# Performance work log

Hardware: AMD Instinct MI355X
Metric: run time of the kernel (lower is better)

## Reference

```python
import jax, jax.numpy as jnp
import numpy as np

N_NODES = 100000
N_EDGES = 1600000
IN_C = 128
HID = 128
LAT = 64
N_LAYERS = 3
N_GRAPHS = 1000


def setup_inputs() -> dict:
    key = jax.random.key(0)
    ks = jax.random.split(key, 16)
    x = jax.random.normal(ks[0], (N_NODES, IN_C), dtype=jnp.float32)
    edge_index = jax.random.randint(ks[1], (2, N_EDGES), 0, N_NODES, dtype=jnp.int64)
    batch = jnp.sort(jax.random.randint(ks[2], (N_NODES,), 0, N_GRAPHS, dtype=jnp.int64))
    s = 1.0 / np.sqrt(HID)
    # per-layer GIN MLP params (in_c == hidden for all layers since IN_C == HID)
    W1 = jax.random.normal(ks[3], (N_LAYERS, IN_C, HID), dtype=jnp.float32) * s
    b1 = jnp.zeros((N_LAYERS, HID), dtype=jnp.float32)
    W2 = jax.random.normal(ks[4], (N_LAYERS, HID, HID), dtype=jnp.float32) * s
    b2 = jnp.zeros((N_LAYERS, HID), dtype=jnp.float32)
    W_mu = jax.random.normal(ks[5], (HID, LAT), dtype=jnp.float32) * s
    b_mu = jnp.zeros((LAT,), dtype=jnp.float32)
    W_lv = jax.random.normal(ks[6], (HID, LAT), dtype=jnp.float32) * s
    b_lv = jnp.zeros((LAT,), dtype=jnp.float32)
    return {"x": x, "edge_index": edge_index, "batch": batch,
            "W1": W1, "b1": b1, "W2": W2, "b2": b2,
            "W_mu": W_mu, "b_mu": b_mu, "W_lv": W_lv, "b_lv": b_lv}


def reference(x, edge_index, batch, W1, b1, W2, b2, W_mu, b_mu, W_lv, b_lv):
    src, dst = edge_index[0], edge_index[1]
    h = x
    for i in range(N_LAYERS):
        # GINConv (eps=0): h' = MLP(h + sum_{j in N(i)} h_j); scatter-add over edges
        agg = h + jax.ops.segment_sum(h[src], dst, num_segments=N_NODES)
        h = jax.nn.relu(agg @ W1[i] + b1[i])
        h = jax.nn.relu(h @ W2[i] + b2[i])
        h = jax.nn.relu(h)  # extra ReLU in forward after conv (idempotent here)
    # global_add_pool: segment-sum nodes into graphs
    g = jax.ops.segment_sum(h, batch, num_segments=N_GRAPHS)  # [G, HID]
    mu = g @ W_mu + b_mu
    logvar = g @ W_lv + b_lv
    return (mu, logvar)
```

## Files before the change

kernel.cpp:

```cpp
#include <hip/hip_runtime.h>

#define N_NODES 100000
#define N_EDGES 1600000
#define HID 128
#define LAT 64
#define N_LAYERS 3
#define N_GRAPHS 1000
#define CAP 64
#define NBIN 391
#define MAXBIN 4608
#define ACHUNK 8192
#define ABLOCKS ((N_EDGES + ACHUNK - 1) / ACHUNK)
#define CVT_BLOCKS (N_NODES * HID / 4 / 256)

typedef short bf16x8 __attribute__((ext_vector_type(8)));
typedef float f32x4 __attribute__((ext_vector_type(4)));

__device__ __forceinline__ float bf2f(unsigned short h) {
    union { unsigned int u; float f; } c;
    c.u = ((unsigned int)h) << 16;
    return c.f;
}
__device__ __forceinline__ unsigned short f2bf(float f) {
    union { float f; unsigned int u; } c;
    c.f = f;
    unsigned int u = c.u;
    return (unsigned short)((u + 0x7fffu + ((u >> 16) & 1u)) >> 16);
}
__device__ __forceinline__ unsigned int pack2(float a, float b) {
    return (unsigned int)f2bf(a) | ((unsigned int)f2bf(b) << 16);
}
__device__ __forceinline__ void addrow(float* acc, uint4 w) {
    acc[0] += bf2f((unsigned short)w.x); acc[1] += bf2f((unsigned short)(w.x >> 16));
    acc[2] += bf2f((unsigned short)w.y); acc[3] += bf2f((unsigned short)(w.y >> 16));
    acc[4] += bf2f((unsigned short)w.z); acc[5] += bf2f((unsigned short)(w.z >> 16));
    acc[6] += bf2f((unsigned short)w.w); acc[7] += bf2f((unsigned short)(w.w >> 16));
}

__global__ __launch_bounds__(256) void prep_kernel(const float* __restrict__ x,
                                                   unsigned short* __restrict__ xb,
                                                   const float* __restrict__ W1,
                                                   const float* __restrict__ W2,
                                                   unsigned short* __restrict__ Wt) {
    int blk = blockIdx.x;
    if (blk < 6) {
        const float* W = ((blk & 1) ? W2 : W1) + (size_t)(blk >> 1) * HID * HID;
        unsigned short* D = Wt + (size_t)blk * HID * HID;
        for (int idx = threadIdx.x; idx < HID * HID; idx += 256) {
            int n = idx >> 7, k = idx & 127;
            D[n * HID + k] = f2bf(W[k * HID + n]);
        }
        return;
    }
    int i = (blk - 6) * 256 + threadIdx.x;
    if (i >= N_NODES * HID / 4) return;
    float4 v = ((const float4*)x)[i];
    ((uint2*)xb)[i] = make_uint2(pack2(v.x, v.y), pack2(v.z, v.w));
}

__global__ __launch_bounds__(256) void binA_kernel(const int* __restrict__ ei,
                                                   int* __restrict__ gcnt,
                                                   unsigned int* __restrict__ ebin) {
    __shared__ unsigned int scount[NBIN];
    __shared__ unsigned int sfill[NBIN];
    int t = threadIdx.x;
    int base = blockIdx.x * ACHUNK;
    int n = N_EDGES - base;
    if (n > ACHUNK) n = ACHUNK;
    for (int i = t; i < NBIN; i += 256) scount[i] = 0u;
    __syncthreads();
    for (int i = t; i < n; i += 256) {
        int d = ei[N_EDGES + base + i];
        atomicAdd(&scount[d >> 8], 1u);
    }
    __syncthreads();
    for (int b = t; b < NBIN; b += 256) {
        unsigned int c = scount[b];
        sfill[b] = c ? (unsigned int)atomicAdd(&gcnt[b], (int)c) : 0u;
    }
    __syncthreads();
    for (int i = t; i < n; i += 256) {
        int s = ei[base + i];
        int d = ei[N_EDGES + base + i];
        int b = d >> 8;
        unsigned int pos = atomicAdd(&sfill[b], 1u);
        ebin[(size_t)b * MAXBIN + pos] = ((unsigned int)(d & 255) << 24) | (unsigned int)s;
    }
}

__global__ __launch_bounds__(256) void binB_kernel(const unsigned int* __restrict__ ebin,
                                                   const int* __restrict__ gcnt,
                                                   int* __restrict__ cnt,
                                                   int* __restrict__ csr) {
    __shared__ int scnt[256];
    int b = blockIdx.x;
    int t = threadIdx.x;
    scnt[t] = 0;
    __syncthreads();
    int n0 = b << 8;
    int c = gcnt[b];
    const unsigned int* src = ebin + (size_t)b * MAXBIN;
    for (int i = t; i < c; i += 256) {
        unsigned int e = src[i];
        int dl = (int)(e >> 24);
        int slot = atomicAdd(&scnt[dl], 1);
        csr[(size_t)(n0 + dl) * CAP + slot] = (int)(e & 0xFFFFFFu);
    }
    __syncthreads();
    int node = n0 + t;
    if (node < N_NODES) cnt[node] = scnt[t];
}

__global__ __launch_bounds__(256) void fused_kernel(const unsigned short* __restrict__ h,
                                                    const int* __restrict__ cnt,
                                                    const int* __restrict__ csr,
                                                    const unsigned short* __restrict__ W1t,
                                                    const float* __restrict__ b1,
                                                    const unsigned short* __restrict__ W2t,
                                                    const float* __restrict__ b2,
                                                    unsigned short* __restrict__ out,
                                                    const int* __restrict__ batch,
                                                    float* __restrict__ gpool) {
    __shared__ unsigned short sA[64][136];
    __shared__ unsigned short sW[128][40];
    __shared__ float sb[128];
    __shared__ int sbatch[64];
    const int t = threadIdx.x;
    const int w = t >> 6;
    const int l = t & 63;
    const int lm = l & 15;
    const int quad = l >> 4;
    const int row0 = blockIdx.x * 64;

    if (gpool && t < 64) {
        int n = row0 + t;
        sbatch[t] = (n < N_NODES) ? batch[n] : -1;
    }

    {
        const int q = t & 15;
        const int g16 = t >> 4;
        for (int r4 = 0; r4 < 4; ++r4) {
            int rloc = (r4 << 4) + g16;
            int node = row0 + rloc;
            float acc[8] = {0.f, 0.f, 0.f, 0.f, 0.f, 0.f, 0.f, 0.f};
            if (node < N_NODES) {
                addrow(acc, *(const uint4*)(h + (size_t)node * HID + q * 8));
                const int* nl = csr + (size_t)node * CAP;
                int deg = cnt[node];
                int e = 0;
                for (; e + 8 <= deg; e += 8) {
                    int s0 = nl[e], s1 = nl[e + 1], s2 = nl[e + 2], s3 = nl[e + 3];
                    int s4 = nl[e + 4], s5 = nl[e + 5], s6 = nl[e + 6], s7 = nl[e + 7];
                    uint4 w0 = *(const uint4*)(h + (size_t)s0 * HID + q * 8);
                    uint4 w1 = *(const uint4*)(h + (size_t)s1 * HID + q * 8);
                    uint4 w2 = *(const uint4*)(h + (size_t)s2 * HID + q * 8);
                    uint4 w3 = *(const uint4*)(h + (size_t)s3 * HID + q * 8);
                    uint4 w4 = *(const uint4*)(h + (size_t)s4 * HID + q * 8);
                    uint4 w5 = *(const uint4*)(h + (size_t)s5 * HID + q * 8);
                    uint4 w6 = *(const uint4*)(h + (size_t)s6 * HID + q * 8);
                    uint4 w7 = *(const uint4*)(h + (size_t)s7 * HID + q * 8);
                    addrow(acc, w0); addrow(acc, w1); addrow(acc, w2); addrow(acc, w3);
                    addrow(acc, w4); addrow(acc, w5); addrow(acc, w6); addrow(acc, w7);
                }
                for (; e + 4 <= deg; e += 4) {
                    int s0 = nl[e], s1 = nl[e + 1], s2 = nl[e + 2], s3 = nl[e + 3];
                    uint4 w0 = *(const uint4*)(h + (size_t)s0 * HID + q * 8);
                    uint4 w1 = *(const uint4*)(h + (size_t)s1 * HID + q * 8);
                    uint4 w2 = *(const uint4*)(h + (size_t)s2 * HID + q * 8);
                    uint4 w3 = *(const uint4*)(h + (size_t)s3 * HID + q * 8);
                    addrow(acc, w0); addrow(acc, w1); addrow(acc, w2); addrow(acc, w3);
                }
                for (; e < deg; ++e) {
                    addrow(acc, *(const uint4*)(h + (size_t)nl[e] * HID + q * 8));
                }
            }
            uint4 o;
            o.x = pack2(acc[0], acc[1]);
            o.y = pack2(acc[2], acc[3]);
            o.z = pack2(acc[4], acc[5]);
            o.w = pack2(acc[6], acc[7]);
            *(uint4*)&sA[rloc][q * 8] = o;
        }
    }

    const unsigned short* Wt[2] = {W1t, W2t};
    const float* bias[2] = {b1, b2};

    for (int p = 0; p < 2; ++p) {
        if (t < 128) sb[t] = bias[p][t];
        f32x4 acc[8];
#pragma unroll
        for (int nt = 0; nt < 8; ++nt) acc[nt] = (f32x4){0.f, 0.f, 0.f, 0.f};

        for (int kc = 0; kc < 4; ++kc) {
            __syncthreads();
            for (int idx = t; idx < 512; idx += 256) {
                int n = idx >> 2, kq = idx & 3;
                *(uint4*)&sW[n][kq * 8] =
                    *(const uint4*)(Wt[p] + (size_t)n * HID + kc * 32 + kq * 8);
            }
            __syncthreads();
            bf16x8 a = *(const bf16x8*)&sA[w * 16 + lm][kc * 32 + quad * 8];
#pragma unroll
            for (int nt = 0; nt < 8; ++nt) {
                bf16x8 b = *(const bf16x8*)&sW[nt * 16 + lm][quad * 8];
                acc[nt] = __builtin_amdgcn_mfma_f32_16x16x32_bf16(a, b, acc[nt], 0, 0, 0);
            }
        }
        __syncthreads();
#pragma unroll
        for (int nt = 0; nt < 8; ++nt) {
            float bv = sb[nt * 16 + lm];
#pragma unroll
            for (int r = 0; r < 4; ++r) {
                int m = w * 16 + quad * 4 + r;
                float val = fmaxf(acc[nt][r] + bv, 0.f);
                sA[m][nt * 16 + lm] = f2bf(val);
            }
        }
        __syncthreads();
    }

    if (!gpool) {
        for (int idx = t; idx < 1024; idx += 256) {
            int r = idx >> 4, c = idx & 15;
            int grow = row0 + r;
            if (grow < N_NODES)
                *(uint4*)(out + (size_t)grow * HID + c * 8) = *(const uint4*)&sA[r][c * 8];
        }
    } else {
        int c = t & 127;
        int r0 = (t >> 7) * 32;
        float acc = 0.f;
        int cur = sbatch[r0];
        for (int r = r0; r < r0 + 32; ++r) {
            int b = sbatch[r];
            if (b < 0) break;
            if (b != cur) {
                atomicAdd(&gpool[(size_t)cur * HID + c], acc);
                acc = 0.f;
                cur = b;
            }
            acc += bf2f(sA[r][c]);
        }
        if (cur >= 0) atomicAdd(&gpool[(size_t)cur * HID + c], acc);
    }
}

__global__ __launch_bounds__(128) void head_kernel(const float* __restrict__ g,
                                                   const float* __restrict__ Wmu,
                                                   const float* __restrict__ bmu,
                                                   const float* __restrict__ Wlv,
                                                   const float* __restrict__ blv,
                                                   float* __restrict__ out) {
    __shared__ float sg[HID];
    int gi = blockIdx.x;
    sg[threadIdx.x] = g[(size_t)gi * HID + threadIdx.x];
    __syncthreads();
    int j = threadIdx.x & 63;
    bool is_lv = threadIdx.x >= 64;
    const float* W = is_lv ? Wlv : Wmu;
    float acc = is_lv ? blv[j] : bmu[j];
    for (int k = 0; k < HID; ++k) acc = fmaf(sg[k], W[k * LAT + j], acc);
    out[(is_lv ? (size_t)N_GRAPHS * LAT : 0) + (size_t)gi * LAT + j] = acc;
}

extern "C" void kernel_launch(void* const* d_in, const int* in_sizes, int n_in,
                              void* d_out, int out_size, void* d_ws, size_t ws_size,
                              hipStream_t stream) {
    const float* x     = (const float*)d_in[0];
    const int*   ei    = (const int*)d_in[1];
    const int*   batch = (const int*)d_in[2];
    const float* W1    = (const float*)d_in[3];
    const float* b1    = (const float*)d_in[4];
    const float* W2    = (const float*)d_in[5];
    const float* b2    = (const float*)d_in[6];
    const float* Wmu   = (const float*)d_in[7];
    const float* bmu   = (const float*)d_in[8];
    const float* Wlv   = (const float*)d_in[9];
    const float* blv   = (const float*)d_in[10];
    float* out = (float*)d_out;

    unsigned short* xb   = (unsigned short*)d_ws;
    unsigned short* h1   = xb + (size_t)N_NODES * HID;
    unsigned short* h2   = h1 + (size_t)N_NODES * HID;
    int* csr = (int*)(h2 + (size_t)N_NODES * HID);
    unsigned int* ebin = (unsigned int*)(csr + (size_t)N_NODES * CAP);
    unsigned short* Wt = (unsigned short*)(ebin + (size_t)NBIN * MAXBIN);
    float* g  = (float*)(Wt + (size_t)6 * HID * HID);
    int* gcnt = (int*)(g + (size_t)N_GRAPHS * HID);
    int* cnt  = gcnt + NBIN + 1;

    hipMemsetAsync(g, 0, (size_t)N_GRAPHS * HID * sizeof(float) + (NBIN + 1) * sizeof(int),
                   stream);

    binA_kernel<<<ABLOCKS, 256, 0, stream>>>(ei, gcnt, ebin);
    binB_kernel<<<NBIN, 256, 0, stream>>>(ebin, gcnt, cnt, csr);

    prep_kernel<<<CVT_BLOCKS + 6, 256, 0, stream>>>(x, xb, W1, W2, Wt);

    const unsigned short* hcur = xb;
    unsigned short* hdst = h1;
    for (int i = 0; i < N_LAYERS; ++i) {
        bool last = (i == N_LAYERS - 1);
        fused_kernel<<<(N_NODES + 63) / 64, 256, 0, stream>>>(
            hcur, cnt, csr,
            Wt + (size_t)(2 * i) * HID * HID, b1 + (size_t)i * HID,
            Wt + (size_t)(2 * i + 1) * HID * HID, b2 + (size_t)i * HID,
            hdst, batch, last ? g : nullptr);
        hcur = hdst;
        hdst = (hdst == h1) ? h2 : h1;
    }
    head_kernel<<<N_GRAPHS, 128, 0, stream>>>(g, Wmu, bmu, Wlv, blv, out);
}
```

Before: 454.5 us.

## Shrink fused GIN tile to 16 rows, read weights from global, merge setup kernels

The fused aggregation+MLP kernel now handles 16 nodes per block instead of 64. Each wave computes two 16-column output tiles and loads its MFMA B fragments straight from global/L2, dropping the shared-memory weight staging and most barriers. This gives far more blocks for latency hiding in the gather phase, at the cost of more redundant weight reads per node. Separately, the prep (conversion/transpose) work is folded into the edge-binning kernel launch to save one launch and let the two run concurrently.

```diff
diff --git a/kernel.cpp b/kernel.cpp
--- a/kernel.cpp
+++ b/kernel.cpp
@@ -37,34 +37,36 @@
     acc[6] += bf2f((unsigned short)w.w); acc[7] += bf2f((unsigned short)(w.w >> 16));
 }
 
-__global__ __launch_bounds__(256) void prep_kernel(const float* __restrict__ x,
-                                                   unsigned short* __restrict__ xb,
-                                                   const float* __restrict__ W1,
-                                                   const float* __restrict__ W2,
-                                                   unsigned short* __restrict__ Wt) {
-    int blk = blockIdx.x;
-    if (blk < 6) {
-        const float* W = ((blk & 1) ? W2 : W1) + (size_t)(blk >> 1) * HID * HID;
-        unsigned short* D = Wt + (size_t)blk * HID * HID;
-        for (int idx = threadIdx.x; idx < HID * HID; idx += 256) {
-            int n = idx >> 7, k = idx & 127;
-            D[n * HID + k] = f2bf(W[k * HID + n]);
-        }
-        return;
-    }
-    int i = (blk - 6) * 256 + threadIdx.x;
-    if (i >= N_NODES * HID / 4) return;
-    float4 v = ((const float4*)x)[i];
-    ((uint2*)xb)[i] = make_uint2(pack2(v.x, v.y), pack2(v.z, v.w));
-}
-
-__global__ __launch_bounds__(256) void binA_kernel(const int* __restrict__ ei,
-                                                   int* __restrict__ gcnt,
-                                                   unsigned int* __restrict__ ebin) {
+__global__ __launch_bounds__(256) void setup_kernel(const int* __restrict__ ei,
+                                                    int* __restrict__ gcnt,
+                                                    unsigned int* __restrict__ ebin,
+                                                    const float* __restrict__ x,
+                                                    unsigned short* __restrict__ xb,
+                                                    const float* __restrict__ W1,
+                                                    const float* __restrict__ W2,
+                                                    unsigned short* __restrict__ Wt) {
     __shared__ unsigned int scount[NBIN];
     __shared__ unsigned int sfill[NBIN];
     int t = threadIdx.x;
-    int base = blockIdx.x * ACHUNK;
+    int blk = blockIdx.x;
+    if (blk >= ABLOCKS) {
+        int b2 = blk - ABLOCKS;
+        if (b2 < 6) {
+            const float* W = ((b2 & 1) ? W2 : W1) + (size_t)(b2 >> 1) * HID * HID;
+            unsigned short* D = Wt + (size_t)b2 * HID * HID;
+            for (int idx = t; idx < HID * HID; idx += 256) {
+                int n = idx >> 7, k = idx & 127;
+                D[n * HID + k] = f2bf(W[k * HID + n]);
+            }
+            return;
+        }
+        int i = (b2 - 6) * 256 + t;
+        if (i >= N_NODES * HID / 4) return;
+        float4 v = ((const float4*)x)[i];
+        ((uint2*)xb)[i] = make_uint2(pack2(v.x, v.y), pack2(v.z, v.w));
+        return;
+    }
+    int base = blk * ACHUNK;
     int n = N_EDGES - base;
     if (n > ACHUNK) n = ACHUNK;
     for (int i = t; i < NBIN; i += 256) scount[i] = 0u;
@@ -121,120 +123,105 @@
                                                     unsigned short* __restrict__ out,
                                                     const int* __restrict__ batch,
                                                     float* __restrict__ gpool) {
-    __shared__ unsigned short sA[64][136];
-    __shared__ unsigned short sW[128][40];
-    __shared__ float sb[128];
-    __shared__ int sbatch[64];
+    __shared__ unsigned short sA[16][136];
+    __shared__ int sbatch[16];
     const int t = threadIdx.x;
     const int w = t >> 6;
     const int l = t & 63;
     const int lm = l & 15;
     const int quad = l >> 4;
-    const int row0 = blockIdx.x * 64;
-
-    if (gpool && t < 64) {
+    const int row0 = blockIdx.x * 16;
+
+    if (gpool && t < 16) {
         int n = row0 + t;
         sbatch[t] = (n < N_NODES) ? batch[n] : -1;
     }
 
     {
         const int q = t & 15;
-        const int g16 = t >> 4;
-        for (int r4 = 0; r4 < 4; ++r4) {
-            int rloc = (r4 << 4) + g16;
-            int node = row0 + rloc;
-            float acc[8] = {0.f, 0.f, 0.f, 0.f, 0.f, 0.f, 0.f, 0.f};
-            if (node < N_NODES) {
-                addrow(acc, *(const uint4*)(h + (size_t)node * HID + q * 8));
-                const int* nl = csr + (size_t)node * CAP;
-                int deg = cnt[node];
-                int e = 0;
-                for (; e + 8 <= deg; e += 8) {
-                    int s0 = nl[e], s1 = nl[e + 1], s2 = nl[e + 2], s3 = nl[e + 3];
-                    int s4 = nl[e + 4], s5 = nl[e + 5], s6 = nl[e + 6], s7 = nl[e + 7];
-                    uint4 w0 = *(const uint4*)(h + (size_t)s0 * HID + q * 8);
-                    uint4 w1 = *(const uint4*)(h + (size_t)s1 * HID + q * 8);
-                    uint4 w2 = *(const uint4*)(h + (size_t)s2 * HID + q * 8);
-                    uint4 w3 = *(const uint4*)(h + (size_t)s3 * HID + q * 8);
-                    uint4 w4 = *(const uint4*)(h + (size_t)s4 * HID + q * 8);
-                    uint4 w5 = *(const uint4*)(h + (size_t)s5 * HID + q * 8);
-                    uint4 w6 = *(const uint4*)(h + (size_t)s6 * HID + q * 8);
-                    uint4 w7 = *(const uint4*)(h + (size_t)s7 * HID + q * 8);
-                    addrow(acc, w0); addrow(acc, w1); addrow(acc, w2); addrow(acc, w3);
-                    addrow(acc, w4); addrow(acc, w5); addrow(acc, w6); addrow(acc, w7);
-                }
-                for (; e + 4 <= deg; e += 4) {
-                    int s0 = nl[e], s1 = nl[e + 1], s2 = nl[e + 2], s3 = nl[e + 3];
-                    uint4 w0 = *(const uint4*)(h + (size_t)s0 * HID + q * 8);
-                    uint4 w1 = *(const uint4*)(h + (size_t)s1 * HID + q * 8);
-                    uint4 w2 = *(const uint4*)(h + (size_t)s2 * HID + q * 8);
-                    uint4 w3 = *(const uint4*)(h + (size_t)s3 * HID + q * 8);
-                    addrow(acc, w0); addrow(acc, w1); addrow(acc, w2); addrow(acc, w3);
-                }
-                for (; e < deg; ++e) {
-                    addrow(acc, *(const uint4*)(h + (size_t)nl[e] * HID + q * 8));
-                }
-            }
-            uint4 o;
-            o.x = pack2(acc[0], acc[1]);
-            o.y = pack2(acc[2], acc[3]);
-            o.z = pack2(acc[4], acc[5]);
-            o.w = pack2(acc[6], acc[7]);
-            *(uint4*)&sA[rloc][q * 8] = o;
-        }
-    }
-
-    const unsigned short* Wt[2] = {W1t, W2t};
+        const int rloc = t >> 4;
+        int node = row0 + rloc;
+        float acc[8] = {0.f, 0.f, 0.f, 0.f, 0.f, 0.f, 0.f, 0.f};
+        if (node < N_NODES) {
+            addrow(acc, *(const uint4*)(h + (size_t)node * HID + q * 8));
+            const int* nl = csr + (size_t)node * CAP;
+            int deg = cnt[node];
+            int e = 0;
+            for (; e + 8 <= deg; e += 8) {
+                int s0 = nl[e], s1 = nl[e + 1], s2 = nl[e + 2], s3 = nl[e + 3];
+                int s4 = nl[e + 4], s5 = nl[e + 5], s6 = nl[e + 6], s7 = nl[e + 7];
+                uint4 w0 = *(const uint4*)(h + (size_t)s0 * HID + q * 8);
+                uint4 w1 = *(const uint4*)(h + (size_t)s1 * HID + q * 8);
+                uint4 w2 = *(const uint4*)(h + (size_t)s2 * HID + q * 8);
+                uint4 w3 = *(const uint4*)(h + (size_t)s3 * HID + q * 8);
+                uint4 w4 = *(const uint4*)(h + (size_t)s4 * HID + q * 8);
+                uint4 w5 = *(const uint4*)(h + (size_t)s5 * HID + q * 8);
+                uint4 w6 = *(const uint4*)(h + (size_t)s6 * HID + q * 8);
+                uint4 w7 = *(const uint4*)(h + (size_t)s7 * HID + q * 8);
+                addrow(acc, w0); addrow(acc, w1); addrow(acc, w2); addrow(acc, w3);
+                addrow(acc, w4); addrow(acc, w5); addrow(acc, w6); addrow(acc, w7);
+            }
+            for (; e + 4 <= deg; e += 4) {
+                int s0 = nl[e], s1 = nl[e + 1], s2 = nl[e + 2], s3 = nl[e + 3];
+                uint4 w0 = *(const uint4*)(h + (size_t)s0 * HID + q * 8);
+                uint4 w1 = *(const uint4*)(h + (size_t)s1 * HID + q * 8);
+                uint4 w2 = *(const uint4*)(h + (size_t)s2 * HID + q * 8);
+                uint4 w3 = *(const uint4*)(h + (size_t)s3 * HID + q * 8);
+                addrow(acc, w0); addrow(acc, w1); addrow(acc, w2); addrow(acc, w3);
+            }
+            for (; e < deg; ++e) {
+                addrow(acc, *(const uint4*)(h + (size_t)nl[e] * HID + q * 8));
+            }
+        }
+        uint4 o;
+        o.x = pack2(acc[0], acc[1]);
+        o.y = pack2(acc[2], acc[3]);
+        o.z = pack2(acc[4], acc[5]);
+        o.w = pack2(acc[6], acc[7]);
+        *(uint4*)&sA[rloc][q * 8] = o;
+    }
+    __syncthreads();
+
+    const unsigned short* Wt2[2] = {W1t, W2t};
     const float* bias[2] = {b1, b2};
+    const int n0a = (2 * w) * 16 + lm;
+    const int n0b = (2 * w + 1) * 16 + lm;
 
     for (int p = 0; p < 2; ++p) {
-        if (t < 128) sb[t] = bias[p][t];
-        f32x4 acc[8];
+        f32x4 acc0 = (f32x4){0.f, 0.f, 0.f, 0.f};
+        f32x4 acc1 = (f32x4){0.f, 0.f, 0.f, 0.f};
+        const unsigned short* Wp = Wt2[p];
 #pragma unroll
-        for (int nt = 0; nt < 8; ++nt) acc[nt] = (f32x4){0.f, 0.f, 0.f, 0.f};
-
         for (int kc = 0; kc < 4; ++kc) {
-            __syncthreads();
-            for (int idx = t; idx < 512; idx += 256) {
-                int n = idx >> 2, kq = idx & 3;
-                *(uint4*)&sW[n][kq * 8] =
-                    *(const uint4*)(Wt[p] + (size_t)n * HID + kc * 32 + kq * 8);
-            }
-            __syncthreads();
-            bf16x8 a = *(const bf16x8*)&sA[w * 16 + lm][kc * 32 + quad * 8];
+            bf16x8 a = *(const bf16x8*)&sA[lm][kc * 32 + quad * 8];
+            bf16x8 bfr0 = *(const bf16x8*)(Wp + (size_t)n0a * HID + kc * 32 + quad * 8);
+            bf16x8 bfr1 = *(const bf16x8*)(Wp + (size_t)n0b * HID + kc * 32 + quad * 8);
+            acc0 = __builtin_amdgcn_mfma_f32_16x16x32_bf16(a, bfr0, acc0, 0, 0, 0);
+            acc1 = __builtin_amdgcn_mfma_f32_16x16x32_bf16(a, bfr1, acc1, 0, 0, 0);
+        }
+        __syncthreads();
+        float bv0 = bias[p][n0a];
+        float bv1 = bias[p][n0b];
 #pragma unroll
-            for (int nt = 0; nt < 8; ++nt) {
-                bf16x8 b = *(const bf16x8*)&sW[nt * 16 + lm][quad * 8];
-                acc[nt] = __builtin_amdgcn_mfma_f32_16x16x32_bf16(a, b, acc[nt], 0, 0, 0);
-            }
+        for (int r = 0; r < 4; ++r) {
+            int m = quad * 4 + r;
+            sA[m][n0a] = f2bf(fmaxf(acc0[r] + bv0, 0.f));
+            sA[m][n0b] = f2bf(fmaxf(acc1[r] + bv1, 0.f));
         }
         __syncthreads();
-#pragma unroll
-        for (int nt = 0; nt < 8; ++nt) {
-            float bv = sb[nt * 16 + lm];
-#pragma unroll
-            for (int r = 0; r < 4; ++r) {
-                int m = w * 16 + quad * 4 + r;
-                float val = fmaxf(acc[nt][r] + bv, 0.f);
-                sA[m][nt * 16 + lm] = f2bf(val);
-            }
-        }
-        __syncthreads();
     }
 
     if (!gpool) {
-        for (int idx = t; idx < 1024; idx += 256) {
-            int r = idx >> 4, c = idx & 15;
-            int grow = row0 + r;
-            if (grow < N_NODES)
-                *(uint4*)(out + (size_t)grow * HID + c * 8) = *(const uint4*)&sA[r][c * 8];
-        }
+        int r = t >> 4, c = t & 15;
+        int grow = row0 + r;
+        if (grow < N_NODES)
+            *(uint4*)(out + (size_t)grow * HID + c * 8) = *(const uint4*)&sA[r][c * 8];
     } else {
         int c = t & 127;
-        int r0 = (t >> 7) * 32;
+        int r0 = (t >> 7) * 8;
         float acc = 0.f;
         int cur = sbatch[r0];
-        for (int r = r0; r < r0 + 32; ++r) {
+        for (int r = r0; r < r0 + 8; ++r) {
             int b = sbatch[r];
             if (b < 0) break;
             if (b != cur) {
@@ -295,16 +282,15 @@
     hipMemsetAsync(g, 0, (size_t)N_GRAPHS * HID * sizeof(float) + (NBIN + 1) * sizeof(int),
                    stream);
 
-    binA_kernel<<<ABLOCKS, 256, 0, stream>>>(ei, gcnt, ebin);
+    setup_kernel<<<ABLOCKS + 6 + CVT_BLOCKS, 256, 0, stream>>>(ei, gcnt, ebin,
+                                                               x, xb, W1, W2, Wt);
     binB_kernel<<<NBIN, 256, 0, stream>>>(ebin, gcnt, cnt, csr);
-
-    prep_kernel<<<CVT_BLOCKS + 6, 256, 0, stream>>>(x, xb, W1, W2, Wt);
 
     const unsigned short* hcur = xb;
     unsigned short* hdst = h1;
     for (int i = 0; i < N_LAYERS; ++i) {
         bool last = (i == N_LAYERS - 1);
-        fused_kernel<<<(N_NODES + 63) / 64, 256, 0, stream>>>(
+        fused_kernel<<<(N_NODES + 15) / 16, 256, 0, stream>>>(
             hcur, cnt, csr,
             Wt + (size_t)(2 * i) * HID * HID, b1 + (size_t)i * HID,
             Wt + (size_t)(2 * i + 1) * HID * HID, b2 + (size_t)i * HID,
```

New measurement: 428.8 us. -5.7%, faster.
